# Performance work log

Measured on AMD Instinct MI355X. Metric: run time of the kernel, lower is better.

The kernel has to match this reference:

```python
import jax, jax.numpy as jnp
import numpy as np

T, B, H = 2048, 8, 16
KF, VF, KS, VS = 32, 64, 128, 64


def _l2norm(x, eps=1e-6):
    return x / jnp.sqrt(jnp.sum(x * x, axis=-1, keepdims=True) + eps)


def setup_inputs() -> dict:
    key = jax.random.key(0)
    ks = jax.random.split(key, 12)
    # k/q are L2-normalized externally (per E88/E90 kernel contract)
    k_fast = _l2norm(jax.random.normal(ks[0], (T, B, H, KF), jnp.float32))
    q_fast = _l2norm(jax.random.normal(ks[1], (T, B, H, KF), jnp.float32))
    v_fast = jax.random.normal(ks[2], (T, B, H, VF), jnp.float32)
    k_slow = _l2norm(jax.random.normal(ks[3], (T, B, H, KS), jnp.float32))
    q_slow = _l2norm(jax.random.normal(ks[4], (T, B, H, KS), jnp.float32))
    v_slow = jax.random.normal(ks[5], (T, B, H, VS), jnp.float32)
    # decay factors in (0.85, 1.0): typical Mamba2-style per-head scalar decay
    decay_fast = 0.85 + 0.15 * jax.random.uniform(ks[6], (T, B, H), jnp.float32)
    decay_slow = 0.85 + 0.15 * jax.random.uniform(ks[7], (T, B, H), jnp.float32)
    slow_gate = jax.random.uniform(ks[8], (T, B, H), jnp.float32)
    mix_fast = jax.random.uniform(ks[9], (T, B, H), jnp.float32)
    mix_slow = jax.random.uniform(ks[10], (T, B, H), jnp.float32)
    S_fast0 = jnp.zeros((B, H, KF, VF), jnp.float32)
    S_slow0 = jnp.zeros((B, H, KS, VS), jnp.float32)
    return dict(k_fast=k_fast, v_fast=v_fast, q_fast=q_fast, decay_fast=decay_fast,
                k_slow=k_slow, v_slow=v_slow, q_slow=q_slow, decay_slow=decay_slow,
                slow_gate=slow_gate, mix_fast=mix_fast, mix_slow=mix_slow,
                S_fast0=S_fast0, S_slow0=S_slow0, n_heads=H)


def _e90_scan(k_fast, v_fast, q_fast, decay_fast,
              k_slow, v_slow, q_slow, decay_slow,
              slow_gate, mix_fast, mix_slow, S_fast0, S_slow0):
    def step(carry, x):
        S_f, S_s = carry  # [B,H,KF,VF], [B,H,KS,VS]
        kf, vf, qf, df, ksl, vsl, qsl, dsl, g, mf, ms = x
        # fast state: updated every timestep (decay + rank-1 outer product)
        S_f = df[..., None, None] * S_f + kf[..., :, None] * vf[..., None, :]
        # slow state: gated soft update
        S_s_new = dsl[..., None, None] * S_s + ksl[..., :, None] * vsl[..., None, :]
        g_ = g[..., None, None]
        S_s = g_ * S_s_new + (1.0 - g_) * S_s
        out_f = jnp.einsum('bhk,bhkv->bhv', qf, S_f)
        out_s = jnp.einsum('bhk,bhkv->bhv', qsl, S_s)
        out = mf[..., None] * out_f + ms[..., None] * out_s
        return (S_f, S_s), out

    xs = (k_fast, v_fast, q_fast, decay_fast,
          k_slow, v_slow, q_slow, decay_slow,
          slow_gate, mix_fast, mix_slow)
    (S_f_final, S_s_final), output = jax.lax.scan(step, (S_fast0, S_slow0), xs)
    return S_f_final, S_s_final, output  # output: [T,B,H,VF]


def reference(k_fast, v_fast, q_fast, decay_fast, k_slow, v_slow, q_slow,
              decay_slow, slow_gate, mix_fast, mix_slow, S_fast0, S_slow0, n_heads):
    return _e90_scan(k_fast, v_fast, q_fast, decay_fast,
                     k_slow, v_slow, q_slow, decay_slow,
                     slow_gate, mix_fast, mix_slow, S_fast0, S_slow0)
```

## Files before the change

### kernel.cpp

```cpp
#include <hip/hip_runtime.h>

#define T_STEPS 2048
#define BH      128
#define KS_     128
#define VS_     64
#define KF_     32
#define VF_     64
#define LCH     32
#define NCG     32
#define NC      (T_STEPS / LCH)
#define HALF_T  1024
#define NTHR    512
#define WSLOT   5120
#define SCLS_OFF 1310720
#define SCLF_OFF 1835008
#define RUN_OFF  2359296
#define WS_NEEDED_BYTES ((size_t)(RUN_OFF + 512) * 4)
#define SOFF    (BH*KF_*VF_)
#define YOFF    (BH*KF_*VF_ + BH*KS_*VS_)

typedef __attribute__((ext_vector_type(8))) short short8;
typedef __attribute__((ext_vector_type(16))) float f32x16;

#define MFMA32(a,b,c) __builtin_amdgcn_mfma_f32_32x32x16_bf16((a),(b),(c),0,0,0)
#define CROW(r,hi) (((r)&3) + 8*((r)>>2) + 4*(hi))

#define BARRIER_LDS() do {                                    \
    asm volatile("s_waitcnt lgkmcnt(0)" ::: "memory");        \
    __builtin_amdgcn_s_barrier();                             \
    __builtin_amdgcn_sched_barrier(0);                        \
    } while (0)

__device__ __forceinline__ unsigned short f2b(float x) {
    union { float f; unsigned u; } v; v.f = x;
    unsigned r = v.u + 0x7FFFu + ((v.u >> 16) & 1u);
    return (unsigned short)(r >> 16);
}
__device__ __forceinline__ unsigned cvtpk(float lo, float hi_) {
    unsigned r;
    asm("v_cvt_pk_bf16_f32 %0, %1, %2" : "=v"(r) : "v"(lo), "v"(hi_));
    return r;
}
__device__ __forceinline__ short8 ld8(const unsigned short* p) {
    return *(const short8*)p;
}

__global__ __launch_bounds__(NTHR, 2)
void e90_scan(const float* __restrict__ k_fast,  const float* __restrict__ v_fast,
              const float* __restrict__ q_fast,  const float* __restrict__ decay_fast,
              const float* __restrict__ k_slow,  const float* __restrict__ v_slow,
              const float* __restrict__ q_slow,  const float* __restrict__ decay_slow,
              const float* __restrict__ slow_gate, const float* __restrict__ mix_fast,
              const float* __restrict__ mix_slow, const float* __restrict__ S_fast0,
              const float* __restrict__ S_slow0, float* __restrict__ dout,
              float* __restrict__ dws)
{
    __shared__ __align__(16) unsigned short Qs  [2][LCH][136];
    __shared__ __align__(16) unsigned short Ksl [2][LCH][136];
    __shared__ __align__(16) unsigned short Sbs [2][LCH][136];
    __shared__ __align__(16) unsigned short Psl [2][LCH][40];
    __shared__ __align__(16) unsigned short Pfl [2][LCH][40];
    __shared__ __align__(16) unsigned short Qfl [2][LCH][40];
    __shared__ __align__(16) unsigned short Kfl [2][LCH][40];
    __shared__ __align__(16) unsigned short Sbfl[2][LCH][40];
    __shared__ __align__(16) unsigned short VTs [2][2][LCH][40];
    __shared__ __align__(16) unsigned short VTf [2][2][LCH][40];

    const int tid  = threadIdx.x;
    const int th   = tid >> 8;
    const int gtid = tid & 255;
    const int wid4 = ((tid >> 6) + (th << 1)) & 3;
    const int lane = tid & 63;
    const int l31  = lane & 31;
    const int hi   = lane >> 5;
    const int s_   = gtid >> 3;
    const int sub  = gtid & 7;
    const int k0_  = sub * 16;
    const int j0_  = sub * 4;
    const int bid  = blockIdx.x;
    const int xcd  = bid & 7;
    const int jj   = bid >> 3;
    const int p    = xcd * 16 + (jj >> 1);
    const int vh   = jj & 1;
    const int v0   = vh * 32;
    const int slot = p * 2 + vh;
    const int tgb  = th * HALF_T;

    float* out_y = dout + YOFF;

    f32x16 St0, St1, oacc;
#pragma unroll
    for (int r = 0; r < 16; ++r) { St0[r] = 0.0f; St1[r] = 0.0f; oacc[r] = 0.0f; }
    if (th == 0) {
        if (wid4 < 2) {
#pragma unroll
            for (int r = 0; r < 16; ++r) {
                St0[r] = S_slow0[((size_t)p*KS_ + 32*(2*wid4)   + CROW(r,hi))*VS_ + v0 + l31];
                St1[r] = S_slow0[((size_t)p*KS_ + 32*(2*wid4+1) + CROW(r,hi))*VS_ + v0 + l31];
            }
        } else if (wid4 == 2) {
#pragma unroll
            for (int r = 0; r < 16; ++r)
                St0[r] = S_fast0[((size_t)p*KF_ + CROW(r,hi))*VF_ + v0 + l31];
        }
    }
    if (wid4 < 2) {
#pragma unroll
        for (int r = 0; r < 16; ++r) {
            Sbs[th][l31][32*(2*wid4)   + CROW(r,hi)] = f2b(St0[r]);
            Sbs[th][l31][32*(2*wid4+1) + CROW(r,hi)] = f2b(St1[r]);
        }
    } else if (wid4 == 2) {
#pragma unroll
        for (int r = 0; r < 16; ++r) Sbfl[th][l31][CROW(r,hi)] = f2b(St0[r]);
    }

    float4 pK0,pK1,pK2,pK3, pQ0,pQ1,pQ2,pQ3, pVs,pVf,pKf,pQf;
    float pL0 = 0.f, pL1 = 0.f, pL2 = 0.f;

#define LOADCHUNK(CIDX) do {                                                    \
    int tc_ = (CIDX); if (tc_ > NCG-1) tc_ = NCG-1;                             \
    const int tb_ = tgb + tc_ * LCH;                                            \
    const float* bk_ = k_slow + ((size_t)(tb_+s_)*BH + p)*KS_ + k0_;            \
    pK0 = *(const float4*)bk_;      pK1 = *(const float4*)(bk_+4);              \
    pK2 = *(const float4*)(bk_+8);  pK3 = *(const float4*)(bk_+12);             \
    const float* bq_ = q_slow + ((size_t)(tb_+s_)*BH + p)*KS_ + k0_;            \
    pQ0 = *(const float4*)bq_;      pQ1 = *(const float4*)(bq_+4);              \
    pQ2 = *(const float4*)(bq_+8);  pQ3 = *(const float4*)(bq_+12);             \
    pVs = *(const float4*)(v_slow + ((size_t)(tb_+s_)*BH + p)*VS_ + v0 + j0_);  \
    pVf = *(const float4*)(v_fast + ((size_t)(tb_+s_)*BH + p)*VF_ + v0 + j0_);  \
    pKf = *(const float4*)(k_fast + ((size_t)(tb_+s_)*BH + p)*KF_ + j0_);       \
    pQf = *(const float4*)(q_fast + ((size_t)(tb_+s_)*BH + p)*KF_ + j0_);       \
    const size_t so_ = (size_t)(tb_ + l31)*BH + p;                              \
    pL0 = (hi ? decay_fast : decay_slow)[so_];                                  \
    pL1 = (hi ? mix_fast   : slow_gate )[so_];                                  \
    pL2 = hi ? 0.0f : mix_slow[so_];                                            \
    } while (0)

    LOADCHUNK(0);

    float bls = 1.f, blf = 1.f, ib = 1.f, ibf = 1.f, qsc = 0.f, qfc = 0.f, g_s = 0.f;
    float runAcc = 1.0f;

    for (int c = 0; c < NCG; ++c) {
        const int cb = c & 1;
        if (c > 0) {
            if (wid4 < 2) {
#pragma unroll
                for (int r = 0; r < 16; ++r) {
                    Sbs[th][l31][32*(2*wid4)   + CROW(r,hi)] = f2b(St0[r]);
                    Sbs[th][l31][32*(2*wid4+1) + CROW(r,hi)] = f2b(St1[r]);
                }
            } else if (wid4 == 2) {
#pragma unroll
                for (int r = 0; r < 16; ++r) Sbfl[th][l31][CROW(r,hi)] = f2b(St0[r]);
            } else {
                const int pb = cb ^ 1;
                f32x16 o2;
#pragma unroll
                for (int r = 0; r < 16; ++r) o2[r] = 0.0f;
                const unsigned short* ar = &Psl[th][l31][0];
                const unsigned short* br = &VTs[th][pb][l31][0];
                oacc = MFMA32(ld8(ar + 8*hi),      ld8(br + 8*hi),      oacc);
                oacc = MFMA32(ld8(ar + 16 + 8*hi), ld8(br + 16 + 8*hi), oacc);
                const unsigned short* af = &Pfl[th][l31][0];
                const unsigned short* bf = &VTf[th][pb][l31][0];
                o2 = MFMA32(ld8(af + 8*hi),      ld8(bf + 8*hi),      o2);
                o2 = MFMA32(ld8(af + 16 + 8*hi), ld8(bf + 16 + 8*hi), o2);
#pragma unroll
                for (int r = 0; r < 16; ++r) {
                    int tr = CROW(r,hi);
                    out_y[((size_t)(tgb + (c-1)*LCH + tr)*BH + p)*VF_ + v0 + l31] = oacc[r] + o2[r];
                }
            }
        }
        {
            float a = hi ? pL0 : __builtin_fmaf(pL1, pL0, 1.0f - pL1);
            float b = a;
#pragma unroll
            for (int d = 1; d < 32; d <<= 1) {
                float y = __shfl_up(b, d, 32);
                if (l31 >= d) b *= y;
            }
            if (th == 1 && wid4 == 0) {
                float sc = (hi ? pL1 : pL2) * b * runAcc;
                float* wsp = dws + (hi ? SCLF_OFF : SCLS_OFF) + (size_t)slot*HALF_T + c*LCH + l31;
                *wsp = sc;
            }
            float bs_s = __shfl(b, s_);
            float bf_s = __shfl(b, 32 + s_);
            bls = __shfl(b, 31);
            blf = __shfl(b, 63);
            g_s = __shfl(pL1, s_);
            float mf_s = __shfl(pL1, 32 + s_);
            float ms_s = __shfl(pL2, s_);
            ib  = 1.0f / bs_s;
            ibf = 1.0f / bf_s;
            qsc = ms_s * bs_s;
            qfc = mf_s * bf_s;
            runAcc *= (hi ? blf : bls);
        }
        {
            uint4 kw0, kw1, qw0, qw1;
            kw0.x = cvtpk(pK0.x*ib, pK0.y*ib);  kw0.y = cvtpk(pK0.z*ib, pK0.w*ib);
            kw0.z = cvtpk(pK1.x*ib, pK1.y*ib);  kw0.w = cvtpk(pK1.z*ib, pK1.w*ib);
            kw1.x = cvtpk(pK2.x*ib, pK2.y*ib);  kw1.y = cvtpk(pK2.z*ib, pK2.w*ib);
            kw1.z = cvtpk(pK3.x*ib, pK3.y*ib);  kw1.w = cvtpk(pK3.z*ib, pK3.w*ib);
            qw0.x = cvtpk(pQ0.x*qsc, pQ0.y*qsc); qw0.y = cvtpk(pQ0.z*qsc, pQ0.w*qsc);
            qw0.z = cvtpk(pQ1.x*qsc, pQ1.y*qsc); qw0.w = cvtpk(pQ1.z*qsc, pQ1.w*qsc);
            qw1.x = cvtpk(pQ2.x*qsc, pQ2.y*qsc); qw1.y = cvtpk(pQ2.z*qsc, pQ2.w*qsc);
            qw1.z = cvtpk(pQ3.x*qsc, pQ3.y*qsc); qw1.w = cvtpk(pQ3.z*qsc, pQ3.w*qsc);
            *(uint4*)&Ksl[th][s_][k0_]   = kw0;
            *(uint4*)&Ksl[th][s_][k0_+8] = kw1;
            *(uint4*)&Qs [th][s_][k0_]   = qw0;
            *(uint4*)&Qs [th][s_][k0_+8] = qw1;

            VTs[th][cb][j0_+0][s_] = f2b(g_s*pVs.x);
            VTs[th][cb][j0_+1][s_] = f2b(g_s*pVs.y);
            VTs[th][cb][j0_+2][s_] = f2b(g_s*pVs.z);
            VTs[th][cb][j0_+3][s_] = f2b(g_s*pVs.w);
            VTf[th][cb][j0_+0][s_] = f2b(pVf.x);
            VTf[th][cb][j0_+1][s_] = f2b(pVf.y);
            VTf[th][cb][j0_+2][s_] = f2b(pVf.z);
            VTf[th][cb][j0_+3][s_] = f2b(pVf.w);
            uint2 kf2; kf2.x = cvtpk(pKf.x*ibf, pKf.y*ibf); kf2.y = cvtpk(pKf.z*ibf, pKf.w*ibf);
            *(uint2*)&Kfl[th][s_][j0_] = kf2;
            uint2 qf2; qf2.x = cvtpk(pQf.x*qfc, pQf.y*qfc); qf2.y = cvtpk(pQf.z*qfc, pQf.w*qfc);
            *(uint2*)&Qfl[th][s_][j0_] = qf2;
        }
        BARRIER_LDS();

        LOADCHUNK(c + 1);

        if (wid4 < 2) {
            const unsigned short* bv = &VTs[th][cb][l31][0];
            short8 b1 = ld8(bv + 8*hi);
            short8 b2 = ld8(bv + 16 + 8*hi);
            {
                const int T = 2*wid4;
                short8 a1, a2;
#pragma unroll
                for (int e = 0; e < 8; ++e) {
                    a1[e] = (short)Ksl[th][8*hi + e][32*T + l31];
                    a2[e] = (short)Ksl[th][16 + 8*hi + e][32*T + l31];
                }
                St0 = MFMA32(a1, b1, St0);
                St0 = MFMA32(a2, b2, St0);
#pragma unroll
                for (int r = 0; r < 16; ++r) St0[r] *= bls;
            }
            {
                const int T = 2*wid4 + 1;
                short8 a1, a2;
#pragma unroll
                for (int e = 0; e < 8; ++e) {
                    a1[e] = (short)Ksl[th][8*hi + e][32*T + l31];
                    a2[e] = (short)Ksl[th][16 + 8*hi + e][32*T + l31];
                }
                St1 = MFMA32(a1, b1, St1);
                St1 = MFMA32(a2, b2, St1);
#pragma unroll
                for (int r = 0; r < 16; ++r) St1[r] *= bls;
            }
        } else if (wid4 == 2) {
            {
                short8 a1, a2;
#pragma unroll
                for (int e = 0; e < 8; ++e) {
                    a1[e] = (short)Kfl[th][8*hi + e][l31];
                    a2[e] = (short)Kfl[th][16 + 8*hi + e][l31];
                }
                const unsigned short* bv = &VTf[th][cb][l31][0];
                St0 = MFMA32(a1, ld8(bv + 8*hi),      St0);
                St0 = MFMA32(a2, ld8(bv + 16 + 8*hi), St0);
#pragma unroll
                for (int r = 0; r < 16; ++r) St0[r] *= blf;
            }
            {
                f32x16 p1;
#pragma unroll
                for (int r = 0; r < 16; ++r) p1[r] = 0.0f;
                const unsigned short* ar = &Qfl[th][l31][0];
                const unsigned short* br = &Kfl[th][l31][0];
                p1 = MFMA32(ld8(ar + 8*hi),      ld8(br + 8*hi),      p1);
                p1 = MFMA32(ld8(ar + 16 + 8*hi), ld8(br + 16 + 8*hi), p1);
#pragma unroll
                for (int r = 0; r < 16; ++r) {
                    int tr = CROW(r,hi);
                    Pfl[th][tr][l31] = f2b(tr >= l31 ? p1[r] : 0.0f);
                }
            }
            {
                f32x16 p1, p2;
#pragma unroll
                for (int r = 0; r < 16; ++r) { p1[r] = 0.0f; p2[r] = 0.0f; }
                const unsigned short* ar = &Qs [th][l31][0];
                const unsigned short* br = &Ksl[th][l31][0];
                const int kb = 8*hi;
#pragma unroll
                for (int st = 0; st < 8; st += 2) {
                    p1 = MFMA32(ld8(ar + kb + 16*st),     ld8(br + kb + 16*st),     p1);
                    p2 = MFMA32(ld8(ar + kb + 16*(st+1)), ld8(br + kb + 16*(st+1)), p2);
                }
#pragma unroll
                for (int r = 0; r < 16; ++r) {
                    int tr = CROW(r,hi);
                    Psl[th][tr][l31] = f2b(tr >= l31 ? p1[r] + p2[r] : 0.0f);
                }
            }
        } else {
            f32x16 o1, o2;
#pragma unroll
            for (int r = 0; r < 16; ++r) { o1[r] = 0.0f; o2[r] = 0.0f; }
            const unsigned short* ar = &Qs [th][l31][0];
            const unsigned short* br = &Sbs[th][l31][0];
            const int kb = 8*hi;
#pragma unroll
            for (int st = 0; st < 8; st += 2) {
                o1 = MFMA32(ld8(ar + kb + 16*st),     ld8(br + kb + 16*st),     o1);
                o2 = MFMA32(ld8(ar + kb + 16*(st+1)), ld8(br + kb + 16*(st+1)), o2);
            }
            const unsigned short* af = &Qfl [th][l31][0];
            const unsigned short* bf = &Sbfl[th][l31][0];
            o1 = MFMA32(ld8(af + 8*hi),      ld8(bf + 8*hi),      o1);
            o2 = MFMA32(ld8(af + 16 + 8*hi), ld8(bf + 16 + 8*hi), o2);
#pragma unroll
            for (int r = 0; r < 16; ++r) oacc[r] = o1[r] + o2[r];
        }
        BARRIER_LDS();
    }

    if (wid4 == 3) {
        const int pb = (NCG - 1) & 1;
        f32x16 o2;
#pragma unroll
        for (int r = 0; r < 16; ++r) o2[r] = 0.0f;
        const unsigned short* ar = &Psl[th][l31][0];
        const unsigned short* br = &VTs[th][pb][l31][0];
        oacc = MFMA32(ld8(ar + 8*hi),      ld8(br + 8*hi),      oacc);
        oacc = MFMA32(ld8(ar + 16 + 8*hi), ld8(br + 16 + 8*hi), oacc);
        const unsigned short* af = &Pfl[th][l31][0];
        const unsigned short* bf = &VTf[th][pb][l31][0];
        o2 = MFMA32(ld8(af + 8*hi),      ld8(bf + 8*hi),      o2);
        o2 = MFMA32(ld8(af + 16 + 8*hi), ld8(bf + 16 + 8*hi), o2);
#pragma unroll
        for (int r = 0; r < 16; ++r) {
            int tr = CROW(r,hi);
            out_y[((size_t)(tgb + (NCG-1)*LCH + tr)*BH + p)*VF_ + v0 + l31] = oacc[r] + o2[r];
        }
    }

    if (th == 0) {
        if (wid4 < 2) {
#pragma unroll
            for (int r = 0; r < 16; ++r) {
                int cr = CROW(r,hi);
                dout[SOFF + ((size_t)p*KS_ + 32*(2*wid4)   + cr)*VS_ + v0 + l31] = St0[r];
                dout[SOFF + ((size_t)p*KS_ + 32*(2*wid4+1) + cr)*VS_ + v0 + l31] = St1[r];
            }
        } else if (wid4 == 2) {
#pragma unroll
            for (int r = 0; r < 16; ++r)
                dout[((size_t)p*KF_ + CROW(r,hi))*VF_ + v0 + l31] = St0[r];
        }
    } else {
        if (wid4 < 2) {
#pragma unroll
            for (int r = 0; r < 16; ++r) {
                int cr = CROW(r,hi);
                dws[(size_t)slot*WSLOT + (32*(2*wid4)   + cr)*32 + l31] = St0[r];
                dws[(size_t)slot*WSLOT + (32*(2*wid4+1) + cr)*32 + l31] = St1[r];
            }
        } else if (wid4 == 2) {
#pragma unroll
            for (int r = 0; r < 16; ++r)
                dws[(size_t)slot*WSLOT + (128 + CROW(r,hi))*32 + l31] = St0[r];
        }
        if (wid4 == 0 && lane == 0)  dws[RUN_OFF + slot*2 + 0] = runAcc;
        if (wid4 == 0 && lane == 32) dws[RUN_OFF + slot*2 + 1] = runAcc;
    }
#undef LOADCHUNK
}

__global__ __launch_bounds__(NTHR, 2)
void e90_fix(const float* __restrict__ q_fast, const float* __restrict__ q_slow,
             const float* __restrict__ dws, float* __restrict__ dout)
{
    __shared__ __align__(16) unsigned short SbS[32][136];
    __shared__ __align__(16) unsigned short SbF[32][40];

    const int tid  = threadIdx.x;
    const int bid  = blockIdx.x;
    const int xcd  = bid & 7;
    const int jj   = bid >> 3;
    const int p    = xcd * 16 + (jj >> 1);
    const int vh   = jj & 1;
    const int v0   = vh * 32;
    const int slot = p * 2 + vh;
    const int lane = tid & 63;
    const int w8   = tid >> 6;
    const int l31  = lane & 31;
    const int hi   = lane >> 5;

    float* out_y = dout + YOFF;

    for (int i = tid; i < 128 * 32; i += NTHR) {
        int k = i >> 5, v = i & 31;
        SbS[v][k] = f2b(dout[SOFF + ((size_t)p*KS_ + k)*VS_ + v0 + v]);
    }
    for (int i = tid; i < 32 * 32; i += NTHR) {
        int k = i >> 5, v = i & 31;
        SbF[v][k] = f2b(dout[((size_t)p*KF_ + k)*VF_ + v0 + v]);
    }
    __syncthreads();

    {
        const float runS = dws[RUN_OFF + slot*2 + 0];
        const float runF = dws[RUN_OFF + slot*2 + 1];
        for (int i = tid; i < WSLOT; i += NTHR) {
            int k = i >> 5, v = i & 31;
            float st = dws[(size_t)slot*WSLOT + i];
            if (k < 128) {
                size_t o = SOFF + ((size_t)p*KS_ + k)*VS_ + v0 + v;
                dout[o] = runS * dout[o] + st;
            } else {
                size_t o = ((size_t)p*KF_ + (k - 128))*VF_ + v0 + v;
                dout[o] = runF * dout[o] + st;
            }
        }
    }

#pragma unroll 1
    for (int j = 0; j < 4; ++j) {
        const int cc = w8 * 4 + j;
        const int t0 = HALF_T + cc * LCH;
        const float sS = dws[SCLS_OFF + (size_t)slot*HALF_T + cc*LCH + l31];
        const float sF = dws[SCLF_OFF + (size_t)slot*HALF_T + cc*LCH + l31];
        const size_t so = (size_t)(t0 + l31) * BH + p;
        f32x16 c1, c2;
#pragma unroll
        for (int r = 0; r < 16; ++r) { c1[r] = 0.0f; c2[r] = 0.0f; }
#pragma unroll
        for (int st = 0; st < 8; ++st) {
            const float* qp = q_slow + so*KS_ + 16*st + 8*hi;
            float4 x = *(const float4*)qp;
            float4 y = *(const float4*)(qp + 4);
            union { unsigned u[4]; short8 s; } fr;
            fr.u[0] = cvtpk(x.x*sS, x.y*sS);
            fr.u[1] = cvtpk(x.z*sS, x.w*sS);
            fr.u[2] = cvtpk(y.x*sS, y.y*sS);
            fr.u[3] = cvtpk(y.z*sS, y.w*sS);
            if (st & 1) c2 = MFMA32(fr.s, ld8(&SbS[l31][16*st + 8*hi]), c2);
            else        c1 = MFMA32(fr.s, ld8(&SbS[l31][16*st + 8*hi]), c1);
        }
#pragma unroll
        for (int st = 0; st < 2; ++st) {
            const float* qp = q_fast + so*KF_ + 16*st + 8*hi;
            float4 x = *(const float4*)qp;
            float4 y = *(const float4*)(qp + 4);
            union { unsigned u[4]; short8 s; } fr;
            fr.u[0] = cvtpk(x.x*sF, x.y*sF);
            fr.u[1] = cvtpk(x.z*sF, x.w*sF);
            fr.u[2] = cvtpk(y.x*sF, y.y*sF);
            fr.u[3] = cvtpk(y.z*sF, y.w*sF);
            if (st & 1) c2 = MFMA32(fr.s, ld8(&SbF[l31][16*st + 8*hi]), c2);
            else        c1 = MFMA32(fr.s, ld8(&SbF[l31][16*st + 8*hi]), c1);
        }
#pragma unroll
        for (int r = 0; r < 16; ++r) {
            int tr = CROW(r,hi);
            size_t o = ((size_t)(t0 + tr)*BH + p)*VF_ + v0 + l31;
            out_y[o] += c1[r] + c2[r];
        }
    }
}

__global__ __launch_bounds__(NTHR, 2)
void e90_mono(const float* __restrict__ k_fast,  const float* __restrict__ v_fast,
              const float* __restrict__ q_fast,  const float* __restrict__ decay_fast,
              const float* __restrict__ k_slow,  const float* __restrict__ v_slow,
              const float* __restrict__ q_slow,  const float* __restrict__ decay_slow,
              const float* __restrict__ slow_gate, const float* __restrict__ mix_fast,
              const float* __restrict__ mix_slow, const float* __restrict__ S_fast0,
              const float* __restrict__ S_slow0, float* __restrict__ dout)
{
    __shared__ __align__(16) unsigned short Qs  [2][LCH][136];
    __shared__ __align__(16) unsigned short Ksl [2][LCH][136];
    __shared__ __align__(16) unsigned short Sbs [2][LCH][136];
    __shared__ __align__(16) unsigned short Psl [2][LCH][40];
    __shared__ __align__(16) unsigned short Pfl [2][LCH][40];
    __shared__ __align__(16) unsigned short Qfl [2][LCH][40];
    __shared__ __align__(16) unsigned short Kfl [2][LCH][40];
    __shared__ __align__(16) unsigned short Sbfl[2][LCH][40];
    __shared__ __align__(16) unsigned short VTs [3][LCH][40];
    __shared__ __align__(16) unsigned short VTf [3][LCH][40];

    const int tid  = threadIdx.x;
    const int bid  = blockIdx.x;
    const int xcd  = bid & 7;
    const int jj   = bid >> 3;
    const int p    = xcd * 16 + (jj >> 1);
    const int v0   = (jj & 1) * 32;
    const int lane = tid & 63;
    const int wid  = tid >> 6;
    const int l31  = lane & 31;
    const int hi   = lane >> 5;
    const int s_   = tid >> 4;
    const int j0_  = (tid & 15) * 2;
    const int k0_  = (tid & 15) * 8;

    float* out_y = dout + YOFF;

    f32x16 Sst, oacc;
#pragma unroll
    for (int r = 0; r < 16; ++r) { Sst[r] = 0.0f; oacc[r] = 0.0f; }
    if (wid < 4) {
#pragma unroll
        for (int r = 0; r < 16; ++r)
            Sst[r] = S_slow0[((size_t)p*KS_ + 32*wid + CROW(r,hi))*VS_ + v0 + l31];
#pragma unroll
        for (int r = 0; r < 16; ++r) Sbs[0][l31][32*wid + CROW(r,hi)] = f2b(Sst[r]);
    } else if (wid == 4) {
#pragma unroll
        for (int r = 0; r < 16; ++r)
            Sst[r] = S_fast0[((size_t)p*KF_ + CROW(r,hi))*VF_ + v0 + l31];
#pragma unroll
        for (int r = 0; r < 16; ++r) Sbfl[0][l31][CROW(r,hi)] = f2b(Sst[r]);
    }

    float4 pKs0, pKs1, pQs0, pQs1;
    float2 pVs, pVf, pKf, pQf;
    float pL0 = 0.f, pL1 = 0.f, pL2 = 0.f;
    float bls = 1.f, blf = 1.f, ib = 1.f, ibf = 1.f, qsc = 0.f, qfc = 0.f, g_s = 0.f;

#define LOADVEC(CIDX) do {                                                     \
    int tc_ = (CIDX); if (tc_ > NC-1) tc_ = NC-1;                              \
    const int tb_ = tc_ * LCH;                                                 \
    const float* bk_ = k_slow + ((size_t)(tb_+s_)*BH + p)*KS_ + k0_;           \
    pKs0 = *(const float4*)bk_;  pKs1 = *(const float4*)(bk_+4);               \
    const float* bq_ = q_slow + ((size_t)(tb_+s_)*BH + p)*KS_ + k0_;           \
    pQs0 = *(const float4*)bq_;  pQs1 = *(const float4*)(bq_+4);               \
    pVs = *(const float2*)(v_slow + ((size_t)(tb_+s_)*BH + p)*VS_ + v0 + j0_); \
    pVf = *(const float2*)(v_fast + ((size_t)(tb_+s_)*BH + p)*VF_ + v0 + j0_); \
    pKf = *(const float2*)(k_fast + ((size_t)(tb_+s_)*BH + p)*KF_ + j0_);      \
    pQf = *(const float2*)(q_fast + ((size_t)(tb_+s_)*BH + p)*KF_ + j0_);      \
    } while (0)

#define LOADSCL(CIDX) do {                                                     \
    int tc_ = (CIDX); if (tc_ > NC-1) tc_ = NC-1;                              \
    const size_t so_ = (size_t)(tc_*LCH + l31)*BH + p;                         \
    pL0 = (hi ? decay_fast : decay_slow)[so_];                                 \
    pL1 = (hi ? mix_fast   : slow_gate )[so_];                                 \
    pL2 = hi ? 0.0f : mix_slow[so_];                                           \
    } while (0)

#define SCAN() do {                                                            \
    float a_ = hi ? pL0 : __builtin_fmaf(pL1, pL0, 1.0f - pL1);                \
    float b_ = a_;                                                             \
    _Pragma("unroll")                                                          \
    for (int d = 1; d < 32; d <<= 1) {                                         \
        float y_ = __shfl_up(b_, d, 32);                                       \
        if (l31 >= d) b_ *= y_;                                                \
    }                                                                          \
    float bs_s = __shfl(b_, s_);                                               \
    float bf_s = __shfl(b_, 32 + s_);                                          \
    bls = __shfl(b_, 31);                                                      \
    blf = __shfl(b_, 63);                                                      \
    g_s = __shfl(pL1, s_);                                                     \
    float mf_s = __shfl(pL1, 32 + s_);                                         \
    float ms_s = __shfl(pL2, s_);                                              \
    ib  = 1.0f / bs_s;                                                         \
    ibf = 1.0f / bf_s;                                                         \
    qsc = ms_s * bs_s;                                                         \
    qfc = mf_s * bf_s;                                                         \
    } while (0)

#define STAGE(J2, J3) do {                                                     \
    uint4 kw, qw;                                                              \
    kw.x = cvtpk(pKs0.x*ib, pKs0.y*ib);  kw.y = cvtpk(pKs0.z*ib, pKs0.w*ib);   \
    kw.z = cvtpk(pKs1.x*ib, pKs1.y*ib);  kw.w = cvtpk(pKs1.z*ib, pKs1.w*ib);   \
    qw.x = cvtpk(pQs0.x*qsc, pQs0.y*qsc); qw.y = cvtpk(pQs0.z*qsc, pQs0.w*qsc);\
    qw.z = cvtpk(pQs1.x*qsc, pQs1.y*qsc); qw.w = cvtpk(pQs1.z*qsc, pQs1.w*qsc);\
    *(uint4*)&Ksl[J2][s_][k0_] = kw;                                           \
    *(uint4*)&Qs [J2][s_][k0_] = qw;                                           \
    float vt0 = g_s*pVs.x, vt1 = g_s*pVs.y;                                    \
    VTs[J3][j0_  ][s_] = f2b(vt0);                                             \
    VTs[J3][j0_+1][s_] = f2b(vt1);                                             \
    VTf[J3][j0_  ][s_] = f2b(pVf.x);                                           \
    VTf[J3][j0_+1][s_] = f2b(pVf.y);                                           \
    unsigned kfp = cvtpk(pKf.x*ibf, pKf.y*ibf);                                \
    *(unsigned*)&Kfl[J2][s_][j0_] = kfp;                                       \
    unsigned qfp = cvtpk(pQf.x*qfc, pQf.y*qfc);                                \
    *(unsigned*)&Qfl[J2][s_][j0_] = qfp;                                       \
    } while (0)

#define YSTORE(CP) do {                                                        \
    const int p2_ = (CP) & 1, p3_ = (CP) % 3;                                  \
    f32x16 o2;                                                                 \
    _Pragma("unroll")                                                          \
    for (int r = 0; r < 16; ++r) o2[r] = 0.0f;                                 \
    const unsigned short* ar = &Psl[p2_][l31][0];                              \
    const unsigned short* br = &VTs[p3_][l31][0];                              \
    oacc = MFMA32(ld8(ar + 8*hi),      ld8(br + 8*hi),      oacc);             \
    oacc = MFMA32(ld8(ar + 16 + 8*hi), ld8(br + 16 + 8*hi), oacc);             \
    const unsigned short* af = &Pfl[p2_][l31][0];                              \
    const unsigned short* bf = &VTf[p3_][l31][0];                              \
    o2 = MFMA32(ld8(af + 8*hi),      ld8(bf + 8*hi),      o2);                 \
    o2 = MFMA32(ld8(af + 16 + 8*hi), ld8(bf + 16 + 8*hi), o2);                 \
    _Pragma("unroll")                                                          \
    for (int r = 0; r < 16; ++r) {                                             \
        int tr = CROW(r,hi);                                                   \
        out_y[((size_t)((CP)*LCH + tr)*BH + p)*VF_ + v0 + l31] = oacc[r] + o2[r]; \
    }                                                                          \
    } while (0)

    LOADVEC(0);
    LOADSCL(0);
    SCAN();
    LOADSCL(1);
    STAGE(0, 0);
    __syncthreads();

    for (int c = 0; c < NC; ++c) {
        const int i2 = c & 1;
        const int i3 = c % 3;
        LOADVEC(c + 1);

        if (wid < 4) {
            short8 a1, a2;
#pragma unroll
            for (int e = 0; e < 8; ++e) {
                a1[e] = (short)Ksl[i2][8*hi + e][32*wid + l31];
                a2[e] = (short)Ksl[i2][16 + 8*hi + e][32*wid + l31];
            }
            const unsigned short* br = &VTs[i3][l31][0];
            Sst = MFMA32(a1, ld8(br + 8*hi),      Sst);
            Sst = MFMA32(a2, ld8(br + 16 + 8*hi), Sst);
#pragma unroll
            for (int r = 0; r < 16; ++r) Sst[r] *= bls;
        } else if (wid == 4) {
            short8 a1, a2;
#pragma unroll
            for (int e = 0; e < 8; ++e) {
                a1[e] = (short)Kfl[i2][8*hi + e][l31];
                a2[e] = (short)Kfl[i2][16 + 8*hi + e][l31];
            }
            const unsigned short* br = &VTf[i3][l31][0];
            Sst = MFMA32(a1, ld8(br + 8*hi),      Sst);
            Sst = MFMA32(a2, ld8(br + 16 + 8*hi), Sst);
#pragma unroll
            for (int r = 0; r < 16; ++r) Sst[r] *= blf;
        } else if (wid == 5) {
            f32x16 p1, p2;
#pragma unroll
            for (int r = 0; r < 16; ++r) { p1[r] = 0.0f; p2[r] = 0.0f; }
            const unsigned short* ar = &Qs [i2][l31][0];
            const unsigned short* br = &Ksl[i2][l31][0];
            const int kb = 8*hi;
#pragma unroll
            for (int st = 0; st < 8; st += 2) {
                p1 = MFMA32(ld8(ar + kb + 16*st),     ld8(br + kb + 16*st),     p1);
                p2 = MFMA32(ld8(ar + kb + 16*(st+1)), ld8(br + kb + 16*(st+1)), p2);
            }
#pragma unroll
            for (int r = 0; r < 16; ++r) {
                int tr = CROW(r,hi);
                Psl[i2][tr][l31] = f2b(tr >= l31 ? p1[r] + p2[r] : 0.0f);
            }
        } else if (wid == 6) {
            f32x16 p1;
#pragma unroll
            for (int r = 0; r < 16; ++r) p1[r] = 0.0f;
            const unsigned short* ar = &Qfl[i2][l31][0];
            const unsigned short* br = &Kfl[i2][l31][0];
            p1 = MFMA32(ld8(ar + 8*hi),      ld8(br + 8*hi),      p1);
            p1 = MFMA32(ld8(ar + 16 + 8*hi), ld8(br + 16 + 8*hi), p1);
#pragma unroll
            for (int r = 0; r < 16; ++r) {
                int tr = CROW(r,hi);
                Pfl[i2][tr][l31] = f2b(tr >= l31 ? p1[r] : 0.0f);
            }
        } else {
            if (c > 0) YSTORE(c - 1);
            f32x16 o1, o2;
#pragma unroll
            for (int r = 0; r < 16; ++r) { o1[r] = 0.0f; o2[r] = 0.0f; }
            const unsigned short* ar = &Qs [i2][l31][0];
            const unsigned short* br = &Sbs[i2][l31][0];
            const int kb = 8*hi;
#pragma unroll
            for (int st = 0; st < 8; st += 2) {
                o1 = MFMA32(ld8(ar + kb + 16*st),     ld8(br + kb + 16*st),     o1);
                o2 = MFMA32(ld8(ar + kb + 16*(st+1)), ld8(br + kb + 16*(st+1)), o2);
            }
            const unsigned short* af = &Qfl [i2][l31][0];
            const unsigned short* bf = &Sbfl[i2][l31][0];
            o1 = MFMA32(ld8(af + 8*hi),      ld8(bf + 8*hi),      o1);
            o2 = MFMA32(ld8(af + 16 + 8*hi), ld8(bf + 16 + 8*hi), o2);
#pragma unroll
            for (int r = 0; r < 16; ++r) oacc[r] = o1[r] + o2[r];
        }

        SCAN();
        LOADSCL(c + 2);

        if (c < NC - 1) {
            const int j2 = (c + 1) & 1;
            const int j3 = (c + 1) % 3;
            if (wid < 4) {
#pragma unroll
                for (int r = 0; r < 16; ++r) Sbs[j2][l31][32*wid + CROW(r,hi)] = f2b(Sst[r]);
            } else if (wid == 4) {
#pragma unroll
                for (int r = 0; r < 16; ++r) Sbfl[j2][l31][CROW(r,hi)] = f2b(Sst[r]);
            }
            STAGE(j2, j3);
        }
        __syncthreads();
    }

    if (wid == 7) {
        YSTORE(NC - 1);
    }
    if (wid < 4) {
#pragma unroll
        for (int r = 0; r < 16; ++r)
            dout[SOFF + ((size_t)p*KS_ + 32*wid + CROW(r,hi))*VS_ + v0 + l31] = Sst[r];
    } else if (wid == 4) {
#pragma unroll
        for (int r = 0; r < 16; ++r)
            dout[((size_t)p*KF_ + CROW(r,hi))*VF_ + v0 + l31] = Sst[r];
    }
#undef LOADVEC
#undef LOADSCL
#undef SCAN
#undef STAGE
#undef YSTORE
}

extern "C" void kernel_launch(void* const* d_in, const int* in_sizes, int n_in,
                              void* d_out, int out_size, void* d_ws, size_t ws_size,
                              hipStream_t stream)
{
    const float* k_fast     = (const float*)d_in[0];
    const float* v_fast     = (const float*)d_in[1];
    const float* q_fast     = (const float*)d_in[2];
    const float* decay_fast = (const float*)d_in[3];
    const float* k_slow     = (const float*)d_in[4];
    const float* v_slow     = (const float*)d_in[5];
    const float* q_slow     = (const float*)d_in[6];
    const float* decay_slow = (const float*)d_in[7];
    const float* slow_gate  = (const float*)d_in[8];
    const float* mix_fast   = (const float*)d_in[9];
    const float* mix_slow   = (const float*)d_in[10];
    const float* S_fast0    = (const float*)d_in[11];
    const float* S_slow0    = (const float*)d_in[12];
    float* dout = (float*)d_out;
    float* dws  = (float*)d_ws;

    if (ws_size >= WS_NEEDED_BYTES) {
        e90_scan<<<dim3(256), dim3(NTHR), 0, stream>>>(
            k_fast, v_fast, q_fast, decay_fast,
            k_slow, v_slow, q_slow, decay_slow,
            slow_gate, mix_fast, mix_slow, S_fast0, S_slow0, dout, dws);
        e90_fix<<<dim3(256), dim3(NTHR), 0, stream>>>(q_fast, q_slow, dws, dout);
    } else {
        e90_mono<<<dim3(256), dim3(NTHR), 0, stream>>>(
            k_fast, v_fast, q_fast, decay_fast,
            k_slow, v_slow, q_slow, decay_slow,
            slow_gate, mix_fast, mix_slow, S_fast0, S_slow0, dout);
    }
}
```

Baseline: 212.9 us.

## Stage transposed K tiles in LDS for vector MFMA loads and pre-scale V weights

Adds transposed K staging buffers (KT, KTf) loaded straight from global memory, so the state-update MFMA A operands become vectorized 16-byte LDS reads instead of eight scalar strided reads. The decay and gate scaling moves onto new weighted-V buffers (Ws, Wf), with the state decay applied before the MFMA rather than after it. State publication to LDS now uses packed bf16 pair stores. The cost is extra LDS space, more scalar strided global loads in the prefetch, and a per-step reciprocal of the cumulative decay, which can lose precision for long products.

```diff
diff --git a/kernel.cpp b/kernel.cpp
--- a/kernel.cpp
+++ b/kernel.cpp
@@ -65,6 +65,10 @@
     __shared__ __align__(16) unsigned short Sbfl[2][LCH][40];
     __shared__ __align__(16) unsigned short VTs [2][2][LCH][40];
     __shared__ __align__(16) unsigned short VTf [2][2][LCH][40];
+    __shared__ __align__(16) unsigned short KT  [2][KS_][40];
+    __shared__ __align__(16) unsigned short KTf [2][KF_][40];
+    __shared__ __align__(16) unsigned short Ws  [2][LCH][40];
+    __shared__ __align__(16) unsigned short Wf  [2][LCH][40];
 
     const int tid  = threadIdx.x;
     const int th   = tid >> 8;
@@ -77,6 +81,10 @@
     const int sub  = gtid & 7;
     const int k0_  = sub * 16;
     const int j0_  = sub * 4;
+    const int kt_k  = gtid & 127;
+    const int kt_s0 = (gtid >> 7) << 4;
+    const int vt_v  = gtid & 31;
+    const int vt_s0 = (gtid >> 5) << 2;
     const int bid  = blockIdx.x;
     const int xcd  = bid & 7;
     const int jj   = bid >> 3;
@@ -104,18 +112,28 @@
                 St0[r] = S_fast0[((size_t)p*KF_ + CROW(r,hi))*VF_ + v0 + l31];
         }
     }
-    if (wid4 < 2) {
-#pragma unroll
-        for (int r = 0; r < 16; ++r) {
-            Sbs[th][l31][32*(2*wid4)   + CROW(r,hi)] = f2b(St0[r]);
-            Sbs[th][l31][32*(2*wid4+1) + CROW(r,hi)] = f2b(St1[r]);
-        }
-    } else if (wid4 == 2) {
-#pragma unroll
-        for (int r = 0; r < 16; ++r) Sbfl[th][l31][CROW(r,hi)] = f2b(St0[r]);
-    }
-
-    float4 pK0,pK1,pK2,pK3, pQ0,pQ1,pQ2,pQ3, pVs,pVf,pKf,pQf;
+#define PUB_SLOW(TILE, ST) do {                                                \
+    unsigned* prow_ = (unsigned*)&Sbs[th][l31][0];                             \
+    _Pragma("unroll")                                                          \
+    for (int q_ = 0; q_ < 4; ++q_) {                                           \
+        int base_ = (32*(TILE) + 8*q_ + 4*hi) >> 1;                            \
+        prow_[base_ + 0] = cvtpk(ST[4*q_+0], ST[4*q_+1]);                      \
+        prow_[base_ + 1] = cvtpk(ST[4*q_+2], ST[4*q_+3]);                      \
+    } } while (0)
+#define PUB_FAST(ST) do {                                                      \
+    unsigned* prow_ = (unsigned*)&Sbfl[th][l31][0];                            \
+    _Pragma("unroll")                                                          \
+    for (int q_ = 0; q_ < 4; ++q_) {                                           \
+        int base_ = (8*q_ + 4*hi) >> 1;                                        \
+        prow_[base_ + 0] = cvtpk(ST[4*q_+0], ST[4*q_+1]);                      \
+        prow_[base_ + 1] = cvtpk(ST[4*q_+2], ST[4*q_+3]);                      \
+    } } while (0)
+
+    if (wid4 < 2) { PUB_SLOW(2*wid4, St0); PUB_SLOW(2*wid4+1, St1); }
+    else if (wid4 == 2) { PUB_FAST(St0); }
+
+    float4 pK0,pK1,pK2,pK3, pQ0,pQ1,pQ2,pQ3, pKf,pQf;
+    float kvT[16], kfT[4], vsv[4], vfv[4];
     float pL0 = 0.f, pL1 = 0.f, pL2 = 0.f;
 
 #define LOADCHUNK(CIDX) do {                                                    \
@@ -127,10 +145,17 @@
     const float* bq_ = q_slow + ((size_t)(tb_+s_)*BH + p)*KS_ + k0_;            \
     pQ0 = *(const float4*)bq_;      pQ1 = *(const float4*)(bq_+4);              \
     pQ2 = *(const float4*)(bq_+8);  pQ3 = *(const float4*)(bq_+12);             \
-    pVs = *(const float4*)(v_slow + ((size_t)(tb_+s_)*BH + p)*VS_ + v0 + j0_);  \
-    pVf = *(const float4*)(v_fast + ((size_t)(tb_+s_)*BH + p)*VF_ + v0 + j0_);  \
     pKf = *(const float4*)(k_fast + ((size_t)(tb_+s_)*BH + p)*KF_ + j0_);       \
     pQf = *(const float4*)(q_fast + ((size_t)(tb_+s_)*BH + p)*KF_ + j0_);       \
+    _Pragma("unroll")                                                           \
+    for (int i_ = 0; i_ < 16; ++i_)                                             \
+        kvT[i_] = k_slow[((size_t)(tb_+kt_s0+i_)*BH + p)*KS_ + kt_k];           \
+    _Pragma("unroll")                                                           \
+    for (int i_ = 0; i_ < 4; ++i_) {                                            \
+        kfT[i_] = k_fast[((size_t)(tb_+vt_s0+i_)*BH + p)*KF_ + vt_v];           \
+        vsv[i_] = v_slow[((size_t)(tb_+vt_s0+i_)*BH + p)*VS_ + v0 + vt_v];      \
+        vfv[i_] = v_fast[((size_t)(tb_+vt_s0+i_)*BH + p)*VF_ + v0 + vt_v];      \
+    }                                                                           \
     const size_t so_ = (size_t)(tb_ + l31)*BH + p;                              \
     pL0 = (hi ? decay_fast : decay_slow)[so_];                                  \
     pL1 = (hi ? mix_fast   : slow_gate )[so_];                                  \
@@ -139,22 +164,15 @@
 
     LOADCHUNK(0);
 
-    float bls = 1.f, blf = 1.f, ib = 1.f, ibf = 1.f, qsc = 0.f, qfc = 0.f, g_s = 0.f;
+    float bls = 1.f, blf = 1.f, ib = 1.f, ibf = 1.f, qsc = 0.f, qfc = 0.f;
     float runAcc = 1.0f;
 
     for (int c = 0; c < NCG; ++c) {
         const int cb = c & 1;
         if (c > 0) {
-            if (wid4 < 2) {
-#pragma unroll
-                for (int r = 0; r < 16; ++r) {
-                    Sbs[th][l31][32*(2*wid4)   + CROW(r,hi)] = f2b(St0[r]);
-                    Sbs[th][l31][32*(2*wid4+1) + CROW(r,hi)] = f2b(St1[r]);
-                }
-            } else if (wid4 == 2) {
-#pragma unroll
-                for (int r = 0; r < 16; ++r) Sbfl[th][l31][CROW(r,hi)] = f2b(St0[r]);
-            } else {
+            if (wid4 < 2) { PUB_SLOW(2*wid4, St0); PUB_SLOW(2*wid4+1, St1); }
+            else if (wid4 == 2) { PUB_FAST(St0); }
+            else {
                 const int pb = cb ^ 1;
                 f32x16 o2;
 #pragma unroll
@@ -174,6 +192,7 @@
                 }
             }
         }
+        float gob;
         {
             float a = hi ? pL0 : __builtin_fmaf(pL1, pL0, 1.0f - pL1);
             float b = a;
@@ -187,11 +206,11 @@
                 float* wsp = dws + (hi ? SCLF_OFF : SCLS_OFF) + (size_t)slot*HALF_T + c*LCH + l31;
                 *wsp = sc;
             }
+            gob = (hi ? 1.0f : pL1) / b;
             float bs_s = __shfl(b, s_);
             float bf_s = __shfl(b, 32 + s_);
             bls = __shfl(b, 31);
             blf = __shfl(b, 63);
-            g_s = __shfl(pL1, s_);
             float mf_s = __shfl(pL1, 32 + s_);
             float ms_s = __shfl(pL2, s_);
             ib  = 1.0f / bs_s;
@@ -215,66 +234,67 @@
             *(uint4*)&Qs [th][s_][k0_]   = qw0;
             *(uint4*)&Qs [th][s_][k0_+8] = qw1;
 
-            VTs[th][cb][j0_+0][s_] = f2b(g_s*pVs.x);
-            VTs[th][cb][j0_+1][s_] = f2b(g_s*pVs.y);
-            VTs[th][cb][j0_+2][s_] = f2b(g_s*pVs.z);
-            VTs[th][cb][j0_+3][s_] = f2b(g_s*pVs.w);
-            VTf[th][cb][j0_+0][s_] = f2b(pVf.x);
-            VTf[th][cb][j0_+1][s_] = f2b(pVf.y);
-            VTf[th][cb][j0_+2][s_] = f2b(pVf.z);
-            VTf[th][cb][j0_+3][s_] = f2b(pVf.w);
-            uint2 kf2; kf2.x = cvtpk(pKf.x*ibf, pKf.y*ibf); kf2.y = cvtpk(pKf.z*ibf, pKf.w*ibf);
-            *(uint2*)&Kfl[th][s_][j0_] = kf2;
-            uint2 qf2; qf2.x = cvtpk(pQf.x*qfc, pQf.y*qfc); qf2.y = cvtpk(pQf.z*qfc, pQf.w*qfc);
-            *(uint2*)&Qfl[th][s_][j0_] = qf2;
+            float gi0 = __shfl(pL1, vt_s0 + 0), gi1 = __shfl(pL1, vt_s0 + 1);
+            float gi2 = __shfl(pL1, vt_s0 + 2), gi3 = __shfl(pL1, vt_s0 + 3);
+            float ws0 = bls * __shfl(gob, vt_s0 + 0), ws1 = bls * __shfl(gob, vt_s0 + 1);
+            float ws2 = bls * __shfl(gob, vt_s0 + 2), ws3 = bls * __shfl(gob, vt_s0 + 3);
+            float wf0 = blf * __shfl(gob, 32 + vt_s0 + 0), wf1 = blf * __shfl(gob, 32 + vt_s0 + 1);
+            float wf2 = blf * __shfl(gob, 32 + vt_s0 + 2), wf3 = blf * __shfl(gob, 32 + vt_s0 + 3);
+
+            uint2 w2;
+            w2.x = cvtpk(gi0*vsv[0], gi1*vsv[1]); w2.y = cvtpk(gi2*vsv[2], gi3*vsv[3]);
+            *(uint2*)&VTs[th][cb][vt_v][vt_s0] = w2;
+            w2.x = cvtpk(vfv[0], vfv[1]);          w2.y = cvtpk(vfv[2], vfv[3]);
+            *(uint2*)&VTf[th][cb][vt_v][vt_s0] = w2;
+            w2.x = cvtpk(ws0*vsv[0], ws1*vsv[1]);  w2.y = cvtpk(ws2*vsv[2], ws3*vsv[3]);
+            *(uint2*)&Ws[th][vt_v][vt_s0] = w2;
+            w2.x = cvtpk(wf0*vfv[0], wf1*vfv[1]);  w2.y = cvtpk(wf2*vfv[2], wf3*vfv[3]);
+            *(uint2*)&Wf[th][vt_v][vt_s0] = w2;
+            uint4 t4;
+            t4.x = cvtpk(kvT[0], kvT[1]);  t4.y = cvtpk(kvT[2], kvT[3]);
+            t4.z = cvtpk(kvT[4], kvT[5]);  t4.w = cvtpk(kvT[6], kvT[7]);
+            *(uint4*)&KT[th][kt_k][kt_s0] = t4;
+            t4.x = cvtpk(kvT[8], kvT[9]);  t4.y = cvtpk(kvT[10], kvT[11]);
+            t4.z = cvtpk(kvT[12], kvT[13]); t4.w = cvtpk(kvT[14], kvT[15]);
+            *(uint4*)&KT[th][kt_k][kt_s0+8] = t4;
+            w2.x = cvtpk(kfT[0], kfT[1]);  w2.y = cvtpk(kfT[2], kfT[3]);
+            *(uint2*)&KTf[th][vt_v][vt_s0] = w2;
+
+            unsigned kfp = cvtpk(pKf.x*ibf, pKf.y*ibf);
+            unsigned kfp2 = cvtpk(pKf.z*ibf, pKf.w*ibf);
+            *(uint2*)&Kfl[th][s_][j0_] = make_uint2(kfp, kfp2);
+            unsigned qfp = cvtpk(pQf.x*qfc, pQf.y*qfc);
+            unsigned qfp2 = cvtpk(pQf.z*qfc, pQf.w*qfc);
+            *(uint2*)&Qfl[th][s_][j0_] = make_uint2(qfp, qfp2);
         }
         BARRIER_LDS();
 
         LOADCHUNK(c + 1);
 
         if (wid4 < 2) {
-            const unsigned short* bv = &VTs[th][cb][l31][0];
-            short8 b1 = ld8(bv + 8*hi);
-            short8 b2 = ld8(bv + 16 + 8*hi);
+            const unsigned short* bw = &Ws[th][l31][0];
+            short8 b1 = ld8(bw + 8*hi);
+            short8 b2 = ld8(bw + 16 + 8*hi);
+#pragma unroll
+            for (int r = 0; r < 16; ++r) { St0[r] *= bls; St1[r] *= bls; }
             {
-                const int T = 2*wid4;
-                short8 a1, a2;
-#pragma unroll
-                for (int e = 0; e < 8; ++e) {
-                    a1[e] = (short)Ksl[th][8*hi + e][32*T + l31];
-                    a2[e] = (short)Ksl[th][16 + 8*hi + e][32*T + l31];
-                }
-                St0 = MFMA32(a1, b1, St0);
-                St0 = MFMA32(a2, b2, St0);
-#pragma unroll
-                for (int r = 0; r < 16; ++r) St0[r] *= bls;
+                const unsigned short* arow = &KT[th][32*(2*wid4) + l31][0];
+                St0 = MFMA32(ld8(arow + 8*hi),      b1, St0);
+                St0 = MFMA32(ld8(arow + 16 + 8*hi), b2, St0);
             }
             {
-                const int T = 2*wid4 + 1;
-                short8 a1, a2;
-#pragma unroll
-                for (int e = 0; e < 8; ++e) {
-                    a1[e] = (short)Ksl[th][8*hi + e][32*T + l31];
-                    a2[e] = (short)Ksl[th][16 + 8*hi + e][32*T + l31];
-                }
-                St1 = MFMA32(a1, b1, St1);
-                St1 = MFMA32(a2, b2, St1);
-#pragma unroll
-                for (int r = 0; r < 16; ++r) St1[r] *= bls;
+                const unsigned short* arow = &KT[th][32*(2*wid4+1) + l31][0];
+                St1 = MFMA32(ld8(arow + 8*hi),      b1, St1);
+                St1 = MFMA32(ld8(arow + 16 + 8*hi), b2, St1);
             }
         } else if (wid4 == 2) {
             {
-                short8 a1, a2;
-#pragma unroll
-                for (int e = 0; e < 8; ++e) {
-                    a1[e] = (short)Kfl[th][8*hi + e][l31];
-                    a2[e] = (short)Kfl[th][16 + 8*hi + e][l31];
-                }
-                const unsigned short* bv = &VTf[th][cb][l31][0];
-                St0 = MFMA32(a1, ld8(bv + 8*hi),      St0);
-                St0 = MFMA32(a2, ld8(bv + 16 + 8*hi), St0);
 #pragma unroll
                 for (int r = 0; r < 16; ++r) St0[r] *= blf;
+                const unsigned short* arow = &KTf[th][l31][0];
+                const unsigned short* bw = &Wf[th][l31][0];
+                St0 = MFMA32(ld8(arow + 8*hi),      ld8(bw + 8*hi),      St0);
+                St0 = MFMA32(ld8(arow + 16 + 8*hi), ld8(bw + 16 + 8*hi), St0);
             }
             {
                 f32x16 p1;
@@ -380,6 +400,8 @@
         if (wid4 == 0 && lane == 32) dws[RUN_OFF + slot*2 + 1] = runAcc;
     }
 #undef LOADCHUNK
+#undef PUB_SLOW
+#undef PUB_FAST
 }
 
 __global__ __launch_bounds__(NTHR, 2)
```

New measurement: 260.6 us. 1.22x slower.
